# Optimization experiments

Hardware: AMD Instinct MI355X
Metric: run time of the kernel (lower is better)

Reference implementation:

```python
import jax, jax.numpy as jnp
import numpy as np

N = 50000
E = 1600000
D = 64


def setup_inputs() -> dict:
    key = jax.random.key(0)
    ks = jax.random.split(key, 12)
    glorot = lambda k, shape: jax.random.uniform(
        k, shape, jnp.float32, -1.0, 1.0) * (np.sqrt(2.0) * np.sqrt(6.0 / sum(shape)))
    return {
        "feat": jax.random.normal(ks[0], (N, D), jnp.float32),
        "norm": jax.random.uniform(ks[1], (N,), jnp.float32),
        "edge_src": jax.random.randint(ks[2], (E,), 0, N),
        "edge_dst": jax.random.randint(ks[3], (E,), 0, N),
        "etype": jax.random.randint(ks[4], (E,), 0, 4),
        "W_rel": glorot(ks[5], (D, D)),
        "lin_w": glorot(ks[6], (2 * D, 1)),
        "lin_b": jnp.zeros((1,), jnp.float32),
        "loop_w": glorot(ks[7], (D, D)),
        "evolve_loop_w": glorot(ks[8], (D, D)),
    }


def reference(feat, norm, edge_src, edge_dst, etype, W_rel, lin_w, lin_b,
              loop_w, evolve_loop_w):
    # --- message function: per-edge attention + per-edge matmul ---
    src = feat[edge_src]              # [E, D] gather
    dst = feat[edge_dst]              # [E, D] gather
    att_logit = jnp.concatenate([src, dst], axis=1) @ lin_w + lin_b  # [E, 1]
    atten = jax.nn.sigmoid(jax.nn.relu(att_logit[:, 0]))            # [E]
    # source code applies weight_relation to every edge-type bucket, so the
    # etype split+concat is a no-op permutation of messages
    msg = src @ W_rel                                                # [E, D]

    # --- reduce: attention-weighted mailbox sum (segment reduction) ---
    agg = jax.ops.segment_sum(atten[:, None] * msg, edge_dst, num_segments=N)
    indeg = jax.ops.segment_sum(jnp.ones((edge_dst.shape[0],), feat.dtype),
                                edge_dst, num_segments=N)            # [N]
    has_msg = (indeg > 0)[:, None]
    # DGL: zero in-degree nodes keep their old feat; apply_func scales by norm
    node_feat = jnp.where(has_msg, agg, feat) * norm[:, None]

    # --- self loop: loop_weight where in_degree>0, evolve_loop_weight else ---
    loop_msg = jnp.where(has_msg, feat @ loop_w, feat @ evolve_loop_w)

    return jnp.tanh(node_feat + loop_msg)
```

## Files before the change

kernel.cpp:

```cpp
#include <hip/hip_runtime.h>
#include <hip/hip_bf16.h>
#include <hip/hip_fp16.h>
#include <math.h>


#define D 64
#define SHIFT 6
#define NB (1 << SHIFT)
#define SCM 1024
#define CHUNK 2048
#define CAPB 2560
#define NPW 8

typedef _Float16 half8 __attribute__((ext_vector_type(8)));
typedef float f32x4 __attribute__((ext_vector_type(4)));

__global__ __launch_bounds__(256) void fused_pre(
    const float* __restrict__ feat, const float* __restrict__ W_rel,
    const float* __restrict__ lin_w, const float* __restrict__ lin_b,
    const float* __restrict__ loop_w, const float* __restrict__ evolve_w,
    float* __restrict__ s1, float* __restrict__ s2, __half* __restrict__ FWh,
    __half* __restrict__ WT, int N) {
  if (blockIdx.x == 0) {
    for (int i = threadIdx.x; i < 192 * 64; i += 256) {
      const int c192 = i >> 6, k = i & 63;
      const int m = c192 >> 6, c = c192 & 63;
      const float* Wm = (m == 0) ? W_rel : (m == 1) ? loop_w : evolve_w;
      WT[i] = __float2half(Wm[k * 64 + c]);
    }
  }

  const int lane = threadIdx.x & 63;
  const int w    = threadIdx.x >> 6;
  const int r    = lane & 15;
  const int g    = lane >> 4;
  const int m0   = (blockIdx.x * 4 + w) * 16;
  if (m0 >= N) return;

  half8 bw[4][2];
  half8 ba[2];
  #pragma unroll
  for (int ks = 0; ks < 2; ++ks) {
    #pragma unroll
    for (int j = 0; j < 8; ++j) {
      const int k = ks * 32 + g * 8 + j;
      #pragma unroll
      for (int nt = 0; nt < 4; ++nt)
        bw[nt][ks][j] = (_Float16)W_rel[k * 64 + nt * 16 + r];
      const float av = (r == 0) ? lin_w[k] : (r == 1) ? lin_w[64 + k] : 0.0f;
      ba[ks][j] = (_Float16)av;
    }
  }

  half8 ah[2], al[2];
  const int arow = m0 + r;
  #pragma unroll
  for (int ks = 0; ks < 2; ++ks) {
    float v[8];
    if (arow < N) {
      const float4 u0 = *(const float4*)&feat[(size_t)arow * D + ks * 32 + g * 8];
      const float4 u1 = *(const float4*)&feat[(size_t)arow * D + ks * 32 + g * 8 + 4];
      v[0] = u0.x; v[1] = u0.y; v[2] = u0.z; v[3] = u0.w;
      v[4] = u1.x; v[5] = u1.y; v[6] = u1.z; v[7] = u1.w;
    } else {
      #pragma unroll
      for (int q = 0; q < 8; ++q) v[q] = 0.0f;
    }
    #pragma unroll
    for (int q = 0; q < 8; ++q) {
      const _Float16 hh = (_Float16)v[q];
      ah[ks][q] = hh;
      al[ks][q] = (_Float16)(v[q] - (float)hh);
    }
  }

  #pragma unroll
  for (int nt = 0; nt < 4; ++nt) {
    f32x4 acc = {0.0f, 0.0f, 0.0f, 0.0f};
    #pragma unroll
    for (int ks = 0; ks < 2; ++ks) {
      acc = __builtin_amdgcn_mfma_f32_16x16x32_f16(ah[ks], bw[nt][ks], acc, 0, 0, 0);
      acc = __builtin_amdgcn_mfma_f32_16x16x32_f16(al[ks], bw[nt][ks], acc, 0, 0, 0);
    }
    #pragma unroll
    for (int q = 0; q < 4; ++q) {
      const int n = m0 + g * 4 + q;
      if (n < N) FWh[(size_t)n * D + nt * 16 + r] = __float2half(acc[q]);
    }
  }

  f32x4 acc5 = {0.0f, 0.0f, 0.0f, 0.0f};
  #pragma unroll
  for (int ks = 0; ks < 2; ++ks) {
    acc5 = __builtin_amdgcn_mfma_f32_16x16x32_f16(ah[ks], ba[ks], acc5, 0, 0, 0);
    acc5 = __builtin_amdgcn_mfma_f32_16x16x32_f16(al[ks], ba[ks], acc5, 0, 0, 0);
  }
  if (r < 2) {
    const float b = lin_b[0];
    #pragma unroll
    for (int q = 0; q < 4; ++q) {
      const int n = m0 + g * 4 + q;
      if (n < N) {
        if (r == 0) s1[n] = acc5[q] + b;
        else        s2[n] = acc5[q];
      }
    }
  }
}

__global__ __launch_bounds__(512) void coarse_scatter(
    const int* __restrict__ esrc, const int* __restrict__ edst,
    const float* __restrict__ s1, const float* __restrict__ s2,
    int* __restrict__ gcur, uint2* __restrict__ ebuf, int E, int C) {
  __shared__ int h[SCM];
  __shared__ int cur[SCM];
  __shared__ int bl[SCM];
  for (int i = threadIdx.x; i < C; i += 512) h[i] = 0;
  __syncthreads();
  const int E4 = E >> 2;
  const int4* edst4 = (const int4*)edst;
  const int4* esrc4 = (const int4*)esrc;
  const int i4 = blockIdx.x * 512 + threadIdx.x;
  const bool tail0 = (blockIdx.x == 0) && (threadIdx.x == 0);

  if (i4 < E4) {
    const int4 d = edst4[i4];
    atomicAdd(&h[d.x >> SHIFT], 1);
    atomicAdd(&h[d.y >> SHIFT], 1);
    atomicAdd(&h[d.z >> SHIFT], 1);
    atomicAdd(&h[d.w >> SHIFT], 1);
  }
  if (tail0) for (int e = E4 << 2; e < E; ++e) atomicAdd(&h[edst[e] >> SHIFT], 1);
  __syncthreads();
  for (int i = threadIdx.x; i < C; i += 512) {
    const int v = h[i];
    bl[i] = v ? atomicAdd(&gcur[i], v) : 0;
    cur[i] = 0;
  }
  __syncthreads();

  if (i4 < E4) {
    const int4 s = esrc4[i4];
    const int4 d = edst4[i4];
    const int ss[4] = {s.x, s.y, s.z, s.w};
    const int dd[4] = {d.x, d.y, d.z, d.w};
    float a1[4], a2[4];
    #pragma unroll
    for (int j = 0; j < 4; ++j) a1[j] = s1[ss[j]];
    #pragma unroll
    for (int j = 0; j < 4; ++j) a2[j] = s2[dd[j]];
    #pragma unroll
    for (int j = 0; j < 4; ++j) {
      const float a = 1.0f / (1.0f + __expf(-fmaxf(a1[j] + a2[j], 0.0f)));
      const int bk = dd[j] >> SHIFT;
      const int rr = atomicAdd(&cur[bk], 1);
      ebuf[(size_t)bk * CAPB + bl[bk] + rr] =
          make_uint2((unsigned)ss[j] | ((unsigned)(dd[j] & (NB - 1)) << 26),
                     __float_as_uint(a));
    }
  }
  if (tail0) {
    for (int e = E4 << 2; e < E; ++e) {
      const int sj = esrc[e], dj = edst[e];
      const float a = 1.0f / (1.0f + __expf(-fmaxf(s1[sj] + s2[dj], 0.0f)));
      const int bk = dj >> SHIFT;
      const int rr = atomicAdd(&cur[bk], 1);
      ebuf[(size_t)bk * CAPB + bl[bk] + rr] =
          make_uint2((unsigned)sj | ((unsigned)(dj & (NB - 1)) << 26),
                     __float_as_uint(a));
    }
  }
}

__global__ __launch_bounds__(512, 4) void sort_reduce_finalize(
    const float* __restrict__ feat, const __half* __restrict__ FWh,
    const __half* __restrict__ WT, const float* __restrict__ norm,
    const int* __restrict__ gcur, const uint2* __restrict__ ebuf,
    float* __restrict__ out, int C, int N) {
  __shared__ uint2 sdata[CAPB];
  __shared__ float Yl[NB * D];
  __shared__ int hist[NB];
  __shared__ int starts[NB + 1];
  __shared__ int roff[NB];

  const int tid  = threadIdx.x;
  const int lane = tid & 63;
  const int w    = tid >> 6;
  const int b    = blockIdx.x;
  const int n0   = b << SHIFT;
  const int beg  = b * CAPB;
  const int cnt  = min(gcur[b], CAPB);

  if (tid < NB) hist[tid] = 0;
  __syncthreads();

  uint2 ereg[5];
  #pragma unroll
  for (int k = 0; k < 5; ++k) {
    const int i = tid + (k << 9);
    if (i < cnt) {
      ereg[k] = ebuf[beg + i];
      atomicAdd(&hist[ereg[k].x >> 26], 1);
    }
  }
  __syncthreads();
  if (tid < 64) {
    const int v = hist[tid];
    int incl = v;
    #pragma unroll
    for (int off = 1; off < 64; off <<= 1) {
      const int o = __shfl_up(incl, off, 64);
      if (tid >= off) incl += o;
    }
    starts[tid] = incl - v;
    roff[tid]   = incl - v;
    if (tid == 63) starts[64] = incl;
  }
  __syncthreads();
  #pragma unroll
  for (int k = 0; k < 5; ++k) {
    const int i = tid + (k << 9);
    if (i < cnt) {
      const int pos = atomicAdd(&roff[ereg[k].x >> 26], 1);
      sdata[pos] = ereg[k];
    }
  }

  {
    const int r = lane & 15, g = lane >> 4;
    const bool evw = (w >= 4);
    const int mt = w & 3;
    bool skip = false;
    if (evw) {
      const int rr0 = mt * 16;
      const int flag = (lane < 16)
          ? ((starts[rr0 + lane + 1] > starts[rr0 + lane]) ? 1 : 0) : 1;
      skip = (__ballot(flag == 0) == 0ULL);
    }
    if (!skip) {
      half8 ah[2], al[2];
      const int arow = n0 + mt * 16 + r;
      #pragma unroll
      for (int ks = 0; ks < 2; ++ks) {
        float v[8];
        if (arow < N) {
          const float4 u0 = *(const float4*)&feat[(size_t)arow * D + ks * 32 + g * 8];
          const float4 u1 = *(const float4*)&feat[(size_t)arow * D + ks * 32 + g * 8 + 4];
          v[0] = u0.x; v[1] = u0.y; v[2] = u0.z; v[3] = u0.w;
          v[4] = u1.x; v[5] = u1.y; v[6] = u1.z; v[7] = u1.w;
        } else {
          #pragma unroll
          for (int q = 0; q < 8; ++q) v[q] = 0.0f;
        }
        #pragma unroll
        for (int q = 0; q < 8; ++q) {
          const _Float16 hh = (_Float16)v[q];
          ah[ks][q] = hh;
          al[ks][q] = (_Float16)(v[q] - (float)hh);
        }
      }
      const int wrow0 = evw ? 128 : 64;
      #pragma unroll
      for (int nt = 0; nt < 4; ++nt) {
        f32x4 a0 = {0.0f, 0.0f, 0.0f, 0.0f};
        #pragma unroll
        for (int ks = 0; ks < 2; ++ks) {
          const half8 bw = *reinterpret_cast<const half8*>(
              WT + (size_t)(wrow0 + nt * 16 + r) * 64 + ks * 32 + g * 8);
          a0 = __builtin_amdgcn_mfma_f32_16x16x32_f16(ah[ks], bw, a0, 0, 0, 0);
          a0 = __builtin_amdgcn_mfma_f32_16x16x32_f16(al[ks], bw, a0, 0, 0, 0);
        }
        #pragma unroll
        for (int q = 0; q < 4; ++q) {
          const int gr = mt * 16 + g * 4 + q;
          const bool hm = starts[gr + 1] > starts[gr];
          if (evw != hm) Yl[gr * D + nt * 16 + r] = a0[q];
        }
      }
    }
  }
  __syncthreads();

  const int half = lane >> 5;
  const int hc   = lane & 31;
  float agg[NPW];
  #pragma unroll
  for (int j = 0; j < NPW; ++j) agg[j] = 0.0f;
  for (int j = 0; j < NPW; ++j) {
    const int dl = w * NPW + j;
    const int n  = n0 + dl;
    if (n >= N) break;
    const int rb = __builtin_amdgcn_readfirstlane(starts[dl]);
    const int re = __builtin_amdgcn_readfirstlane(starts[dl + 1]);
    float sa = 0.0f, sb = 0.0f;
    int p = rb;
    for (; p + 16 <= re; p += 16) {
      uint2 ee[8];
      #pragma unroll
      for (int q = 0; q < 8; ++q) ee[q] = sdata[p + 2 * q + half];
      #pragma unroll
      for (int q = 0; q < 8; ++q) {
        const uint vv = *(const uint*)(
            FWh + (((size_t)(ee[q].x & 0x03FFFFFFu)) << 6) + (hc << 1));
        const float a = __uint_as_float(ee[q].y);
        const float2 f2 = __half22float2(*(const __half2*)&vv);
        sa += a * f2.x; sb += a * f2.y;
      }
    }
    for (; p < re; p += 2) {
      const int idx = p + half;
      const bool vld = idx < re;
      const uint2 e = sdata[vld ? idx : rb];
      const uint vv = *(const uint*)(
          FWh + (((size_t)(e.x & 0x03FFFFFFu)) << 6) + (hc << 1));
      const float a = vld ? __uint_as_float(e.y) : 0.0f;
      const float2 f2 = __half22float2(*(const __half2*)&vv);
      sa += a * f2.x; sb += a * f2.y;
    }
    sa += __shfl_xor(sa, 32, 64);
    sb += __shfl_xor(sb, 32, 64);
    const float t0 = __shfl(sa, lane >> 1, 64);
    const float t1 = __shfl(sb, lane >> 1, 64);
    agg[j] = (lane & 1) ? t1 : t0;
  }

  for (int j = 0; j < NPW; ++j) {
    const int dl = w * NPW + j;
    const int n  = n0 + dl;
    if (n >= N) break;
    const bool hm = starts[dl + 1] > starts[dl];
    const float nr = norm[n];
    const float base = hm ? agg[j] : feat[(size_t)n * D + lane];
    out[(size_t)n * D + lane] = tanhf(base * nr + Yl[dl * D + lane]);
  }
}

extern "C" void kernel_launch(void* const* d_in, const int* in_sizes, int n_in,
                              void* d_out, int out_size, void* d_ws, size_t ws_size,
                              hipStream_t stream) {
  const float* feat     = (const float*)d_in[0];
  const float* norm     = (const float*)d_in[1];
  const int*   esrc     = (const int*)d_in[2];
  const int*   edst     = (const int*)d_in[3];
  const float* W_rel    = (const float*)d_in[5];
  const float* lin_w    = (const float*)d_in[6];
  const float* lin_b    = (const float*)d_in[7];
  const float* loop_w   = (const float*)d_in[8];
  const float* evolve_w = (const float*)d_in[9];
  float* out = (float*)d_out;

  const int N = in_sizes[1];
  const int E = in_sizes[2];
  const int C = (N + NB - 1) >> SHIFT;

  char* p = (char*)d_ws;
  float*  s1     = (float*)p;   p += (size_t)N * sizeof(float);
  float*  s2     = (float*)p;   p += (size_t)N * sizeof(float);
  int*    gcur   = (int*)p;     p += (size_t)2048 * sizeof(int);
  __half* WT     = (__half*)p;  p += (size_t)192 * 64 * sizeof(__half);
  __half* FWh    = (__half*)p;  p += (size_t)N * D * sizeof(__half);
  uint2*  ebuf   = (uint2*)p;

  const int eblocks = (E + CHUNK - 1) / CHUNK;
  const int mblocks = (N + 63) / 64;

  hipMemsetAsync(gcur, 0, (size_t)C * sizeof(int), stream);
  fused_pre<<<mblocks, 256, 0, stream>>>(feat, W_rel, lin_w, lin_b,
                                         loop_w, evolve_w,
                                         s1, s2, FWh, WT, N);
  coarse_scatter<<<eblocks, 512, 0, stream>>>(esrc, edst, s1, s2, gcur,
                                              ebuf, E, C);
  sort_reduce_finalize<<<C, 512, 0, stream>>>(feat, FWh, WT, norm,
                                              gcur, ebuf, out, C, N);
}
```

Before: 181.9 us.

## Fuse precompute into scatter and defer attention to reduce, halving edge buffer

Merges the node precompute kernel into the edge scatter kernel, so one fewer launch is needed. The scatter now stores only a packed 4-byte src/dst-local word per edge instead of also storing the attention value. The sigmoid attention is recomputed in the reduce kernel from s1[src] and a per-node s2, which trades edge-buffer write/read bandwidth and shared memory for extra gathers and transcendental math in the reduce loop.

```diff
diff --git a/kernel.cpp b/kernel.cpp
--- a/kernel.cpp
+++ b/kernel.cpp
@@ -8,21 +8,27 @@
 #define SHIFT 6
 #define NB (1 << SHIFT)
 #define SCM 1024
-#define CHUNK 2048
 #define CAPB 2560
 #define NPW 8
 
 typedef _Float16 half8 __attribute__((ext_vector_type(8)));
 typedef float f32x4 __attribute__((ext_vector_type(4)));
 
-__global__ __launch_bounds__(256) void fused_pre(
+__global__ __launch_bounds__(512) void pre_scatter(
     const float* __restrict__ feat, const float* __restrict__ W_rel,
     const float* __restrict__ lin_w, const float* __restrict__ lin_b,
     const float* __restrict__ loop_w, const float* __restrict__ evolve_w,
+    const int* __restrict__ esrc, const int* __restrict__ edst,
     float* __restrict__ s1, float* __restrict__ s2, __half* __restrict__ FWh,
-    __half* __restrict__ WT, int N) {
+    __half* __restrict__ WT, int* __restrict__ gcur,
+    unsigned* __restrict__ ebuf, int N, int E, int C) {
+  __shared__ int h[SCM];
+  __shared__ int cur[SCM];
+  __shared__ int bl[SCM];
+  for (int i = threadIdx.x; i < C; i += 512) h[i] = 0;
+
   if (blockIdx.x == 0) {
-    for (int i = threadIdx.x; i < 192 * 64; i += 256) {
+    for (int i = threadIdx.x; i < 192 * 64; i += 512) {
       const int c192 = i >> 6, k = i & 63;
       const int m = c192 >> 6, c = c192 & 63;
       const float* Wm = (m == 0) ? W_rel : (m == 1) ? loop_w : evolve_w;
@@ -34,89 +40,81 @@
   const int w    = threadIdx.x >> 6;
   const int r    = lane & 15;
   const int g    = lane >> 4;
-  const int m0   = (blockIdx.x * 4 + w) * 16;
-  if (m0 >= N) return;
-
-  half8 bw[4][2];
-  half8 ba[2];
-  #pragma unroll
-  for (int ks = 0; ks < 2; ++ks) {
-    #pragma unroll
-    for (int j = 0; j < 8; ++j) {
-      const int k = ks * 32 + g * 8 + j;
-      #pragma unroll
-      for (int nt = 0; nt < 4; ++nt)
-        bw[nt][ks][j] = (_Float16)W_rel[k * 64 + nt * 16 + r];
-      const float av = (r == 0) ? lin_w[k] : (r == 1) ? lin_w[64 + k] : 0.0f;
-      ba[ks][j] = (_Float16)av;
-    }
-  }
-
-  half8 ah[2], al[2];
-  const int arow = m0 + r;
-  #pragma unroll
-  for (int ks = 0; ks < 2; ++ks) {
-    float v[8];
-    if (arow < N) {
-      const float4 u0 = *(const float4*)&feat[(size_t)arow * D + ks * 32 + g * 8];
-      const float4 u1 = *(const float4*)&feat[(size_t)arow * D + ks * 32 + g * 8 + 4];
-      v[0] = u0.x; v[1] = u0.y; v[2] = u0.z; v[3] = u0.w;
-      v[4] = u1.x; v[5] = u1.y; v[6] = u1.z; v[7] = u1.w;
-    } else {
-      #pragma unroll
-      for (int q = 0; q < 8; ++q) v[q] = 0.0f;
-    }
-    #pragma unroll
-    for (int q = 0; q < 8; ++q) {
-      const _Float16 hh = (_Float16)v[q];
-      ah[ks][q] = hh;
-      al[ks][q] = (_Float16)(v[q] - (float)hh);
-    }
-  }
-
-  #pragma unroll
-  for (int nt = 0; nt < 4; ++nt) {
-    f32x4 acc = {0.0f, 0.0f, 0.0f, 0.0f};
+  const int m0   = (blockIdx.x * 8 + w) * 16;
+  if (m0 < N) {
+    half8 bw[4][2];
+    half8 ba[2];
     #pragma unroll
     for (int ks = 0; ks < 2; ++ks) {
-      acc = __builtin_amdgcn_mfma_f32_16x16x32_f16(ah[ks], bw[nt][ks], acc, 0, 0, 0);
-      acc = __builtin_amdgcn_mfma_f32_16x16x32_f16(al[ks], bw[nt][ks], acc, 0, 0, 0);
-    }
-    #pragma unroll
-    for (int q = 0; q < 4; ++q) {
-      const int n = m0 + g * 4 + q;
-      if (n < N) FWh[(size_t)n * D + nt * 16 + r] = __float2half(acc[q]);
-    }
-  }
-
-  f32x4 acc5 = {0.0f, 0.0f, 0.0f, 0.0f};
-  #pragma unroll
-  for (int ks = 0; ks < 2; ++ks) {
-    acc5 = __builtin_amdgcn_mfma_f32_16x16x32_f16(ah[ks], ba[ks], acc5, 0, 0, 0);
-    acc5 = __builtin_amdgcn_mfma_f32_16x16x32_f16(al[ks], ba[ks], acc5, 0, 0, 0);
-  }
-  if (r < 2) {
-    const float b = lin_b[0];
-    #pragma unroll
-    for (int q = 0; q < 4; ++q) {
-      const int n = m0 + g * 4 + q;
-      if (n < N) {
-        if (r == 0) s1[n] = acc5[q] + b;
-        else        s2[n] = acc5[q];
-      }
-    }
-  }
-}
-
-__global__ __launch_bounds__(512) void coarse_scatter(
-    const int* __restrict__ esrc, const int* __restrict__ edst,
-    const float* __restrict__ s1, const float* __restrict__ s2,
-    int* __restrict__ gcur, uint2* __restrict__ ebuf, int E, int C) {
-  __shared__ int h[SCM];
-  __shared__ int cur[SCM];
-  __shared__ int bl[SCM];
-  for (int i = threadIdx.x; i < C; i += 512) h[i] = 0;
-  __syncthreads();
+      #pragma unroll
+      for (int j = 0; j < 8; ++j) {
+        const int k = ks * 32 + g * 8 + j;
+        #pragma unroll
+        for (int nt = 0; nt < 4; ++nt)
+          bw[nt][ks][j] = (_Float16)W_rel[k * 64 + nt * 16 + r];
+        const float av = (r == 0) ? lin_w[k] : (r == 1) ? lin_w[64 + k] : 0.0f;
+        ba[ks][j] = (_Float16)av;
+      }
+    }
+
+    half8 ah[2], al[2];
+    const int arow = m0 + r;
+    #pragma unroll
+    for (int ks = 0; ks < 2; ++ks) {
+      float v[8];
+      if (arow < N) {
+        const float4 u0 = *(const float4*)&feat[(size_t)arow * D + ks * 32 + g * 8];
+        const float4 u1 = *(const float4*)&feat[(size_t)arow * D + ks * 32 + g * 8 + 4];
+        v[0] = u0.x; v[1] = u0.y; v[2] = u0.z; v[3] = u0.w;
+        v[4] = u1.x; v[5] = u1.y; v[6] = u1.z; v[7] = u1.w;
+      } else {
+        #pragma unroll
+        for (int q = 0; q < 8; ++q) v[q] = 0.0f;
+      }
+      #pragma unroll
+      for (int q = 0; q < 8; ++q) {
+        const _Float16 hh = (_Float16)v[q];
+        ah[ks][q] = hh;
+        al[ks][q] = (_Float16)(v[q] - (float)hh);
+      }
+    }
+
+    #pragma unroll
+    for (int nt = 0; nt < 4; ++nt) {
+      f32x4 acc = {0.0f, 0.0f, 0.0f, 0.0f};
+      #pragma unroll
+      for (int ks = 0; ks < 2; ++ks) {
+        acc = __builtin_amdgcn_mfma_f32_16x16x32_f16(ah[ks], bw[nt][ks], acc, 0, 0, 0);
+        acc = __builtin_amdgcn_mfma_f32_16x16x32_f16(al[ks], bw[nt][ks], acc, 0, 0, 0);
+      }
+      #pragma unroll
+      for (int q = 0; q < 4; ++q) {
+        const int n = m0 + g * 4 + q;
+        if (n < N) FWh[(size_t)n * D + nt * 16 + r] = __float2half(acc[q]);
+      }
+    }
+
+    f32x4 acc5 = {0.0f, 0.0f, 0.0f, 0.0f};
+    #pragma unroll
+    for (int ks = 0; ks < 2; ++ks) {
+      acc5 = __builtin_amdgcn_mfma_f32_16x16x32_f16(ah[ks], ba[ks], acc5, 0, 0, 0);
+      acc5 = __builtin_amdgcn_mfma_f32_16x16x32_f16(al[ks], ba[ks], acc5, 0, 0, 0);
+    }
+    if (r < 2) {
+      const float b = lin_b[0];
+      #pragma unroll
+      for (int q = 0; q < 4; ++q) {
+        const int n = m0 + g * 4 + q;
+        if (n < N) {
+          if (r == 0) s1[n] = acc5[q] + b;
+          else        s2[n] = acc5[q];
+        }
+      }
+    }
+  }
+
+  __syncthreads();
+
   const int E4 = E >> 2;
   const int4* edst4 = (const int4*)edst;
   const int4* esrc4 = (const int4*)esrc;
@@ -144,30 +142,20 @@
     const int4 d = edst4[i4];
     const int ss[4] = {s.x, s.y, s.z, s.w};
     const int dd[4] = {d.x, d.y, d.z, d.w};
-    float a1[4], a2[4];
-    #pragma unroll
-    for (int j = 0; j < 4; ++j) a1[j] = s1[ss[j]];
-    #pragma unroll
-    for (int j = 0; j < 4; ++j) a2[j] = s2[dd[j]];
     #pragma unroll
     for (int j = 0; j < 4; ++j) {
-      const float a = 1.0f / (1.0f + __expf(-fmaxf(a1[j] + a2[j], 0.0f)));
       const int bk = dd[j] >> SHIFT;
       const int rr = atomicAdd(&cur[bk], 1);
       ebuf[(size_t)bk * CAPB + bl[bk] + rr] =
-          make_uint2((unsigned)ss[j] | ((unsigned)(dd[j] & (NB - 1)) << 26),
-                     __float_as_uint(a));
+          (unsigned)ss[j] | ((unsigned)(dd[j] & (NB - 1)) << 26);
     }
   }
   if (tail0) {
     for (int e = E4 << 2; e < E; ++e) {
-      const int sj = esrc[e], dj = edst[e];
-      const float a = 1.0f / (1.0f + __expf(-fmaxf(s1[sj] + s2[dj], 0.0f)));
-      const int bk = dj >> SHIFT;
+      const int bk = edst[e] >> SHIFT;
       const int rr = atomicAdd(&cur[bk], 1);
       ebuf[(size_t)bk * CAPB + bl[bk] + rr] =
-          make_uint2((unsigned)sj | ((unsigned)(dj & (NB - 1)) << 26),
-                     __float_as_uint(a));
+          (unsigned)esrc[e] | ((unsigned)(edst[e] & (NB - 1)) << 26);
     }
   }
 }
@@ -175,9 +163,10 @@
 __global__ __launch_bounds__(512, 4) void sort_reduce_finalize(
     const float* __restrict__ feat, const __half* __restrict__ FWh,
     const __half* __restrict__ WT, const float* __restrict__ norm,
-    const int* __restrict__ gcur, const uint2* __restrict__ ebuf,
+    const float* __restrict__ s1, const float* __restrict__ s2,
+    const int* __restrict__ gcur, const unsigned* __restrict__ ebuf,
     float* __restrict__ out, int C, int N) {
-  __shared__ uint2 sdata[CAPB];
+  __shared__ unsigned sdata[CAPB];
   __shared__ float Yl[NB * D];
   __shared__ int hist[NB];
   __shared__ int starts[NB + 1];
@@ -194,13 +183,13 @@
   if (tid < NB) hist[tid] = 0;
   __syncthreads();
 
-  uint2 ereg[5];
+  unsigned ereg[5];
   #pragma unroll
   for (int k = 0; k < 5; ++k) {
     const int i = tid + (k << 9);
     if (i < cnt) {
       ereg[k] = ebuf[beg + i];
-      atomicAdd(&hist[ereg[k].x >> 26], 1);
+      atomicAdd(&hist[ereg[k] >> 26], 1);
     }
   }
   __syncthreads();
@@ -221,7 +210,7 @@
   for (int k = 0; k < 5; ++k) {
     const int i = tid + (k << 9);
     if (i < cnt) {
-      const int pos = atomicAdd(&roff[ereg[k].x >> 26], 1);
+      const int pos = atomicAdd(&roff[ereg[k] >> 26], 1);
       sdata[pos] = ereg[k];
     }
   }
@@ -292,30 +281,34 @@
     if (n >= N) break;
     const int rb = __builtin_amdgcn_readfirstlane(starts[dl]);
     const int re = __builtin_amdgcn_readfirstlane(starts[dl + 1]);
+    const float s2n = s2[n];
     float sa = 0.0f, sb = 0.0f;
     int p = rb;
     for (; p + 16 <= re; p += 16) {
-      uint2 ee[8];
+      unsigned ee[8];
       #pragma unroll
       for (int q = 0; q < 8; ++q) ee[q] = sdata[p + 2 * q + half];
       #pragma unroll
       for (int q = 0; q < 8; ++q) {
-        const uint vv = *(const uint*)(
-            FWh + (((size_t)(ee[q].x & 0x03FFFFFFu)) << 6) + (hc << 1));
-        const float a = __uint_as_float(ee[q].y);
+        const unsigned src = ee[q] & 0x03FFFFFFu;
+        const float at = 1.0f / (1.0f + __expf(-fmaxf(s1[src] + s2n, 0.0f)));
+        const unsigned vv = *(const unsigned*)(
+            FWh + (((size_t)src) << 6) + (hc << 1));
         const float2 f2 = __half22float2(*(const __half2*)&vv);
-        sa += a * f2.x; sb += a * f2.y;
+        sa += at * f2.x; sb += at * f2.y;
       }
     }
     for (; p < re; p += 2) {
       const int idx = p + half;
       const bool vld = idx < re;
-      const uint2 e = sdata[vld ? idx : rb];
-      const uint vv = *(const uint*)(
-          FWh + (((size_t)(e.x & 0x03FFFFFFu)) << 6) + (hc << 1));
-      const float a = vld ? __uint_as_float(e.y) : 0.0f;
+      const unsigned e = sdata[vld ? idx : rb];
+      const unsigned src = e & 0x03FFFFFFu;
+      const float at = vld
+          ? 1.0f / (1.0f + __expf(-fmaxf(s1[src] + s2n, 0.0f))) : 0.0f;
+      const unsigned vv = *(const unsigned*)(
+          FWh + (((size_t)src) << 6) + (hc << 1));
       const float2 f2 = __half22float2(*(const __half2*)&vv);
-      sa += a * f2.x; sb += a * f2.y;
+      sa += at * f2.x; sb += at * f2.y;
     }
     sa += __shfl_xor(sa, 32, 64);
     sb += __shfl_xor(sb, 32, 64);
@@ -354,22 +347,21 @@
   const int C = (N + NB - 1) >> SHIFT;
 
   char* p = (char*)d_ws;
-  float*  s1     = (float*)p;   p += (size_t)N * sizeof(float);
-  float*  s2     = (float*)p;   p += (size_t)N * sizeof(float);
-  int*    gcur   = (int*)p;     p += (size_t)2048 * sizeof(int);
-  __half* WT     = (__half*)p;  p += (size_t)192 * 64 * sizeof(__half);
-  __half* FWh    = (__half*)p;  p += (size_t)N * D * sizeof(__half);
-  uint2*  ebuf   = (uint2*)p;
-
-  const int eblocks = (E + CHUNK - 1) / CHUNK;
-  const int mblocks = (N + 63) / 64;
+  float*    s1   = (float*)p;    p += (size_t)N * sizeof(float);
+  float*    s2   = (float*)p;    p += (size_t)N * sizeof(float);
+  int*      gcur = (int*)p;      p += (size_t)2048 * sizeof(int);
+  __half*   WT   = (__half*)p;   p += (size_t)192 * 64 * sizeof(__half);
+  __half*   FWh  = (__half*)p;   p += (size_t)N * D * sizeof(__half);
+  unsigned* ebuf = (unsigned*)p;
+
+  const int E4 = E >> 2;
+  const int eblocks = (E4 + 511) / 512;
 
   hipMemsetAsync(gcur, 0, (size_t)C * sizeof(int), stream);
-  fused_pre<<<mblocks, 256, 0, stream>>>(feat, W_rel, lin_w, lin_b,
-                                         loop_w, evolve_w,
-                                         s1, s2, FWh, WT, N);
-  coarse_scatter<<<eblocks, 512, 0, stream>>>(esrc, edst, s1, s2, gcur,
-                                              ebuf, E, C);
-  sort_reduce_finalize<<<C, 512, 0, stream>>>(feat, FWh, WT, norm,
+  pre_scatter<<<eblocks, 512, 0, stream>>>(feat, W_rel, lin_w, lin_b,
+                                           loop_w, evolve_w, esrc, edst,
+                                           s1, s2, FWh, WT, gcur, ebuf,
+                                           N, E, C);
+  sort_reduce_finalize<<<C, 512, 0, stream>>>(feat, FWh, WT, norm, s1, s2,
                                               gcur, ebuf, out, C, N);
 }
```

Result: slower. 194.3 us (+6.8%).
